# Kernel optimization log

Measured on AMD Instinct MI355X. Metric: run time of the kernel, lower is better.

The kernel has to match this reference:

```python
import jax, jax.numpy as jnp
import numpy as np

# ---- straight-through binary quantizers (custom VJP matches torch autograd.Functions) ----
@jax.custom_vjp
def bq(x):
    return jnp.sign(x)
def _bq_fwd(x):
    return jnp.sign(x), x
def _bq_bwd(x, g):
    return (g * ((x > -1.0) & (x < 1.0)).astype(g.dtype),)
bq.defvjp(_bq_fwd, _bq_bwd)

@jax.custom_vjp
def bq_quad(x):
    return jnp.sign(x)
def _bqq_fwd(x):
    return jnp.sign(x), x
def _bqq_bwd(x, g):
    return (jnp.maximum(2.0 - jnp.abs(2.0 * x), 0.0) * g,)
bq_quad.defvjp(_bqq_fwd, _bqq_bwd)

def bilinear(x, W, s, b):
    # BiLinear: row-centered sign weights scaled by learned per-row factor, sign activations
    Wc = W - jnp.mean(W, axis=-1, keepdims=True)
    Wb = s * bq(Wc)                      # (out, in)
    return bq(x) @ Wb.T + b

def selective_scan(u, delta, A, Bs, Cs, D, delta_bias):
    # u, delta: (B,K,Dn,L); A: (K,Dn,N); Bs,Cs: (B,K,N,L); D, delta_bias: (K,Dn)
    Bn, K, Dn, L = u.shape
    N = A.shape[-1]
    delta = jax.nn.softplus(delta + delta_bias[None, :, :, None])
    def step(h, inp):
        ut, dt, Bt, Ct = inp             # (B,K,Dn),(B,K,Dn),(B,K,N),(B,K,N)
        dA = jnp.exp(dt[..., None] * A[None])
        h = dA * h + (dt * ut)[..., None] * Bt[:, :, None, :]
        y = jnp.einsum('bkdn,bkn->bkd', h, Ct)
        return h, y
    h0 = jnp.zeros((Bn, K, Dn, N), u.dtype)
    _, ys = jax.lax.scan(step, h0,
                         (u.transpose(3, 0, 1, 2), delta.transpose(3, 0, 1, 2),
                          Bs.transpose(3, 0, 1, 2), Cs.transpose(3, 0, 1, 2)))
    y = ys.transpose(1, 2, 3, 0)         # (B,K,Dn,L)
    return y + D[None, :, :, None] * u

def _forward(x, W_in, b_in, s_in, move0_b, conv_W, conv_b, rp_b0, prelu_a, rp_b1,
             Wl, bl, sl, Wd, bd, sd, dt_bias, A_logs, Ds, ln_w, ln_b, W_out, b_out, s_out):
    Bn, H, Wi, dm = x.shape
    Dn = conv_W.shape[0]
    K = 4
    N = A_logs.shape[1]
    R = Wd.shape[2]
    L = H * Wi
    xz = bilinear(x, W_in, s_in, b_in)                  # (B,H,W,2*Dn)
    xp, z = jnp.split(xz, 2, axis=-1)
    xc = xp.transpose(0, 3, 1, 2)                       # (B,Dn,H,W)
    # BConv2d: move0 bias -> sign (quad STE) -> binary conv -> RPReLU -> residual
    t = bq_quad(xc + move0_b[None, :, None, None])
    sc = jax.lax.stop_gradient(jnp.mean(jnp.abs(conv_W), axis=(1, 2, 3), keepdims=True))
    cw = jnp.clip(conv_W, -1.0, 1.0)
    Wb = jax.lax.stop_gradient(sc * jnp.sign(conv_W) - cw) + cw
    t = jax.lax.conv_general_dilated(t, Wb, (1, 1), [(1, 1), (1, 1)],
                                     dimension_numbers=('NCHW', 'OIHW', 'NCHW'))
    t = t + conv_b[None, :, None, None]
    t = t + rp_b0[None, :, None, None]
    t = jnp.where(t >= 0, t, prelu_a[None, :, None, None] * t)
    t = t + rp_b1[None, :, None, None] + xc
    xconv = jax.nn.silu(t)
    # 4-direction scan inputs
    x_flat = xconv.reshape(Bn, Dn, L)
    x_tr = xconv.transpose(0, 1, 3, 2).reshape(Bn, Dn, L)
    x_hwwh = jnp.stack([x_flat, x_tr], axis=1)
    xs = jnp.concatenate([x_hwwh, jnp.flip(x_hwwh, axis=-1)], axis=1)   # (B,K,Dn,L)
    # NOTE: torch does .view(B,L,-1) on contiguous (B,Dn,L) slices = raw reshape (not transpose)
    xin = xs.reshape(Bn, K, L, Dn)
    x_dbl = jax.vmap(bilinear, in_axes=(1, 0, 0, 0), out_axes=1)(xin, Wl, sl, bl)  # (B,K,L,R+2N)
    x_dbl = x_dbl.transpose(0, 1, 3, 2)                                 # (B,K,R+2N,L)
    dts_r, Bs, Cs = jnp.split(x_dbl, [R, R + N], axis=2)
    dts_in = dts_r.reshape(Bn, K, L, R)  # raw reshape, matches torch .view
    dts = jax.vmap(bilinear, in_axes=(1, 0, 0, 0), out_axes=1)(dts_in, Wd, sd, bd)  # (B,K,L,Dn)
    dts = dts.transpose(0, 1, 3, 2)                                     # (B,K,Dn,L)
    A = -jnp.exp(A_logs).reshape(K, Dn, N)
    out_y = selective_scan(xs, dts, A, Bs, Cs, Ds.reshape(K, Dn), dt_bias.reshape(K, Dn))
    inv_y = jnp.flip(out_y[:, 2:4], axis=-1)
    wh_y = out_y[:, 1].reshape(Bn, Dn, Wi, H).transpose(0, 1, 3, 2).reshape(Bn, Dn, L)
    invwh_y = inv_y[:, 1].reshape(Bn, Dn, Wi, H).transpose(0, 1, 3, 2).reshape(Bn, Dn, L)
    y = out_y[:, 0] + inv_y[:, 0] + wh_y + invwh_y                      # (B,Dn,L)
    y = y.transpose(0, 2, 1).reshape(Bn, H, Wi, Dn)
    mu = jnp.mean(y, axis=-1, keepdims=True)
    var = jnp.var(y, axis=-1, keepdims=True)
    y = (y - mu) / jnp.sqrt(var + 1e-5) * ln_w + ln_b                   # LayerNorm eps=1e-5
    y = y * jax.nn.silu(z)
    return bilinear(y, W_out, s_out, b_out)

def setup_inputs():
    key = jax.random.key(0)
    ks = jax.random.split(key, 12)
    B, H, Wi, dm = 4, 64, 64, 96
    Dn, N, R, K = 192, 16, 6, 4
    u = lambda k, sh, a: jax.random.uniform(k, sh, jnp.float32, -a, a)
    x = jax.random.normal(ks[0], (B, H, Wi, dm), jnp.float32)
    W_in = u(ks[1], (2 * Dn, dm), 0.015)
    b_in = u(ks[2], (2 * Dn,), 0.01)
    s_in = jnp.mean(jnp.abs(W_in), axis=1, keepdims=True)
    move0_b = jnp.zeros((Dn,), jnp.float32)
    conv_W = 0.05 * jax.random.normal(ks[3], (Dn, Dn, 3, 3), jnp.float32)
    conv_b = u(ks[4], (Dn,), 0.01)
    rp_b0 = jnp.zeros((Dn,), jnp.float32)
    prelu_a = 0.25 * jnp.ones((Dn,), jnp.float32)
    rp_b1 = jnp.zeros((Dn,), jnp.float32)
    Wl = u(ks[5], (K, R + 2 * N, Dn), 0.015)
    bl = u(ks[6], (K, R + 2 * N), 0.01)
    sl = jnp.mean(jnp.abs(Wl), axis=2, keepdims=True)
    std = R ** -0.5
    Wd = u(ks[7], (K, Dn, R), std)
    bd = u(ks[8], (K, Dn), 0.01)
    sd = jnp.mean(jnp.abs(Wd), axis=2, keepdims=True)
    dt = jnp.exp(jax.random.uniform(ks[9], (K * Dn,), jnp.float32)
                 * (np.log(0.1) - np.log(0.001)) + np.log(0.001))
    dt = jnp.clip(dt, 1e-4, None)
    dt_bias = dt + jnp.log(-jnp.expm1(-dt))
    A_logs = jnp.tile(jnp.log(jnp.arange(1, N + 1, dtype=jnp.float32))[None, :], (K * Dn, 1))
    Ds = jnp.ones((K * Dn,), jnp.float32)
    ln_w = jnp.ones((Dn,), jnp.float32)
    ln_b = jnp.zeros((Dn,), jnp.float32)
    W_out = u(ks[10], (dm, Dn), 0.015)
    b_out = u(ks[11], (dm,), 0.01)
    s_out = jnp.mean(jnp.abs(W_out), axis=1, keepdims=True)
    return dict(x=x, W_in=W_in, b_in=b_in, s_in=s_in, move0_b=move0_b, conv_W=conv_W,
                conv_b=conv_b, rp_b0=rp_b0, prelu_a=prelu_a, rp_b1=rp_b1, Wl=Wl, bl=bl,
                sl=sl, Wd=Wd, bd=bd, sd=sd, dt_bias=dt_bias, A_logs=A_logs, Ds=Ds,
                ln_w=ln_w, ln_b=ln_b, W_out=W_out, b_out=b_out, s_out=s_out)

def reference(x, W_in, b_in, s_in, move0_b, conv_W, conv_b, rp_b0, prelu_a, rp_b1,
              Wl, bl, sl, Wd, bd, sd, dt_bias, A_logs, Ds, ln_w, ln_b, W_out, b_out, s_out):
    return _forward(x, W_in, b_in, s_in, move0_b, conv_W, conv_b, rp_b0, prelu_a, rp_b1,
                    Wl, bl, sl, Wd, bd, sd, dt_bias, A_logs, Ds, ln_w, ln_b, W_out, b_out, s_out)
```

## Files before the change

kernel.cpp:

```cpp
#include <hip/hip_runtime.h>
#include <math.h>
#include <stdint.h>

#define BB 4
#define HH 64
#define WW2 64
#define DM 96
#define DN 192
#define KK 4
#define NN 16
#define RR 6
#define LL 4096
#define RN 38

#define LOG2E 1.4426950408889634f
#define LN2   0.6931471805599453f

#define OFF_WDB      0
#define OFF_WCS      4608
#define OFF_WAUX     15360
#define OFF_WSC      16896
#define OFF_WBIB     17088
#define OFF_WOUTB    18240
#define OFF_WLBB     18816
#define OFF_XBP      19728
#define OFF_PXS      19728
#define OFF_XC       412992
#define OFF_ZS       3558720
#define OFF_XCONV    6704448
#define OFF_XS       9850176
#define OFF_SSUM     22433088
#define OFF_HEND     OFF_XCONV

#define PLANE 4356

__device__ __forceinline__ float fsign(float v) {
  return (v > 0.f) ? 1.f : ((v < 0.f) ? -1.f : 0.f);
}
__device__ __forceinline__ float softplusf(float v) {
  return fmaxf(v, 0.f) + LN2 * log2f(1.f + exp2f(-fabsf(v) * LOG2E));
}
__device__ __forceinline__ float siluf(float v) {
  return v / (1.f + expf(-v));
}
__device__ __forceinline__ float waveAllSum(float s) {
  #pragma unroll
  for (int off = 32; off; off >>= 1) s += __shfl_xor(s, off, 64);
  return s;
}

__global__ __launch_bounds__(64) void k_prep(
    const float* __restrict__ W_in, const float* __restrict__ s_in,
    const float* __restrict__ W_out, const float* __restrict__ s_out,
// ... 100 lines not shown
    uint32_t* plane = (uint32_t*)(ws + OFF_XBP) + (size_t)p * PLANE;
    for (int i = lane; i < 66; i += 64) {
      plane[i] = 0u;
      plane[65 * 66 + i] = 0u;
    }
    for (int i = lane; i < 64; i += 64) {
      plane[(i + 1) * 66] = 0u;
      plane[(i + 1) * 66 + 65] = 0u;
    }
  }
}

__global__ __launch_bounds__(384) void k_bilin_in(
    const float* __restrict__ x, const float* __restrict__ b_in,
    const float* __restrict__ s_in, const float* __restrict__ move0,
    const float* __restrict__ ws, float* __restrict__ xc, float* __restrict__ zs,
    uint32_t* __restrict__ xb) {
  __shared__ uint32_t spx[16 * 3];
  __shared__ float sxz[384 * 17];
  __shared__ float smv[DN];
  int p0 = blockIdx.x * 16;
  if (threadIdx.x < 48) {
    int pix = threadIdx.x / 3, wd = threadIdx.x % 3;
    const float* base = x + (size_t)(p0 + pix) * DM + wd * 32;
    uint32_t wv = 0;
    #pragma unroll
    for (int i = 0; i < 32; ++i) wv |= (base[i] > 0.f ? 1u : 0u) << i;
    spx[pix * 3 + wd] = wv;
  }
  if (threadIdx.x < DN) smv[threadIdx.x] = move0[threadIdx.x];
  __syncthreads();
  int o = threadIdx.x;
  uint32_t w0, w1, w2;
  {
    const uint32_t* wb = (const uint32_t*)(ws + OFF_WBIB) + o * 3;
    w0 = wb[0]; w1 = wb[1]; w2 = wb[2];
  }
  float bias = b_in[o], sc = s_in[o];
  #pragma unroll
  for (int pix = 0; pix < 16; ++pix) {
    int P = (int)__popc(spx[pix * 3 + 0] ^ w0) + (int)__popc(spx[pix * 3 + 1] ^ w1) +
            (int)__popc(spx[pix * 3 + 2] ^ w2);
    sxz[o * 17 + pix] = bias + sc * (float)(DM - 2 * P);
  }
  __syncthreads();
  int b = p0 >> 12, l0 = p0 & 4095;
  for (int f = threadIdx.x; f < DN * 16; f += 384) {
    int od = f >> 4, pix = f & 15;
    xc[((size_t)(b * DN + od)) * LL + l0 + pix] = sxz[od * 17 + pix];
  }
  for (int f = threadIdx.x; f < DN * 16; f += 384) {
    int pix = f / DN, oz = f - pix * DN;
    zs[(size_t)(p0 + pix) * DN + oz] = siluf(sxz[(DN + oz) * 17 + pix]);
  }
  if (threadIdx.x < 96) {
    int pix = threadIdx.x / 6, cw = threadIdx.x % 6;
    uint32_t wv = 0;
    #pragma unroll
    for (int i = 0; i < 32; ++i) {
      int dch = cw * 32 + i;
      wv |= ((sxz[dch * 17 + pix] + smv[dch] > 0.f) ? 1u : 0u) << i;
    }
    int l = l0 + pix, h = l >> 6, w = l & 63;
    uint32_t* plane = xb + (size_t)(b * 6 + cw) * PLANE;
    plane[(h + 1) * 66 + 1 + w] = wv;
  }
}

// ... 59 lines not shown
    }
    if (isB) {
      corr += saux[oc * 8 + 3];
      if (isL) corr -= saux[oc * 8 + 6];
      if (isR) corr -= saux[oc * 8 + 7];
    }
    float acc = sconst[oc * 4 + 0] * (float)(1728 - 2 * P + corr);
    float t = acc + sconst[oc * 4 + 1];
    t = (t >= 0.f) ? t : sconst[oc * 4 + 2] * t;
    t += sconst[oc * 4 + 3] + *xcp;
    *xop = siluf(t);
    xcp += LL; xop += LL;
  }
}

__global__ __launch_bounds__(256) void k_build_xs(const float* __restrict__ xconv,
                                                  float* __restrict__ xs,
                                                  uint32_t* __restrict__ pxs) {
  __shared__ float tile[64][65];
  int bd = blockIdx.x;
  int b = bd / DN, d = bd % DN;
  const float* img = xconv + (size_t)bd * LL;
  for (int i = threadIdx.x; i < LL; i += 256)
    tile[i >> 6][i & 63] = img[i];
  __syncthreads();
  int lane = threadIdx.x & 63;
  #pragma unroll
  for (int k = 0; k < 4; ++k) {
    size_t base = ((size_t)((b * KK + k) * DN + d)) * LL;
    for (int j = threadIdx.x; j < LL; j += 256) {
      float v;
      if (k == 0)      v = tile[j >> 6][j & 63];
      else if (k == 1) v = tile[j & 63][j >> 6];
      else if (k == 2) { int t2 = 4095 - j; v = tile[t2 >> 6][t2 & 63]; }
      else             { int t2 = 4095 - j; v = tile[t2 & 63][t2 >> 6]; }
      xs[base + j] = v;
      unsigned long long m = __ballot(v > 0.f);
      if (lane == 0)       pxs[(base + j) >> 5] = (uint32_t)m;
      else if (lane == 32) pxs[(base + j) >> 5] = (uint32_t)(m >> 32);
    }
  }
}

__device__ __forceinline__ void rpowers(float r, float* a) {
  float r2 = r * r, r3 = r2 * r, r4 = r2 * r2, r8 = r4 * r4;
  a[0] = r;       a[1] = r2;      a[2] = r3;      a[3] = r4;
  a[4] = r4 * r;  a[5] = r4 * r2; a[6] = r4 * r3; a[7] = r8;
  a[8] = r8 * r;  a[9] = r8 * r2; a[10] = r8 * r3; a[11] = r8 * r4;
  a[12] = r8 * a[4]; a[13] = r8 * a[5]; a[14] = r8 * a[6]; a[15] = r8 * r8;
}

__global__ __launch_bounds__(192) void k_scan_a(
    const float* __restrict__ xs, const uint32_t* __restrict__ pxs,
    const float* __restrict__ ws, const float* __restrict__ bl,
    const float* __restrict__ sl, const float* __restrict__ bd,
    const float* __restrict__ dt_bias, const float* __restrict__ A_logs,
    float* __restrict__ hend, float* __restrict__ Ssum) {
  int c = blockIdx.x & 63;
  int bk = blockIdx.x >> 6;
  int k = bk & 3;
  int d = threadIdx.x;
  int t0 = c << 6;
  __shared__ uint32_t sdtm[64];
  __shared__ uint32_t spxr[64 * 6];
  __shared__ uint32_t swl[RN * 6];
  __shared__ float sblv[RN], sslv[RN];
  __shared__ float4 sB4[256];
  __shared__ float sDV[7 * 192], sR[7 * 192];
  float* sBf = (float*)sB4;
  const uint32_t* ppx = pxs + (size_t)bk * 24576;
  for (int i = d; i < 384; i += 192) spxr[i] = ppx[t0 * 6 + i];
  for (int i = d; i < RN * 6; i += 192) swl[i] = ((const uint32_t*)(ws + OFF_WLBB))[k * RN * 6 + i];
  if (d < RN) {
    sblv[d] = bl[k * RN + d];
    sslv[d] = sl[k * RN + d];
  }
  __syncthreads();
  if (d < 64) {
    uint32_t m = 0;
    int fbase = (t0 + d) * 6;
    #pragma unroll
    for (int r = 0; r < 6; ++r) {
      int f = fbase + r;
      int o = f >> 12, l = f & 4095;
      const uint32_t* prow = ppx + l * 6;
      int P = 0;
      #pragma unroll
      for (int j = 0; j < 6; ++j) P += (int)__popc(prow[j] ^ swl[o * 6 + j]);
      float val = sblv[o] + sslv[o] * (float)(DN - 2 * P);
      m |= (val > 0.f ? 1u : 0u) << r;
    }
    sdtm[d] = m;
  }
  for (int i = d; i < 1024; i += 192) {
    int t = i >> 4, n = i & 15;
    int o = RR + n;
    int P = 0;
    #pragma unroll
    for (int j = 0; j < 6; ++j) P += (int)__popc(spxr[t * 6 + j] ^ swl[o * 6 + j]);
    sBf[t * 16 + n] = sblv[o] + sslv[o] * (float)(DN - 2 * P);
  }
  uint32_t w6 = ((const uint32_t*)(ws + OFF_WDB))[k * DN + d];
  float sdv = (ws + OFF_WDB)[768 + k * DN + d];
  float biasd = bd[k * DN + d] + dt_bias[k * DN + d];
  #pragma unroll
  for (int pc = 0; pc < 7; ++pc) {
    float dv = softplusf(biasd + sdv * (float)(RR - 2 * pc));
    sDV[pc * 192 + d] = dv;
    sR[pc * 192 + d] = exp2f(-dv * LOG2E);
  }
  float Araw[16];
  bool fok = true;
  {
    const float* ap = A_logs + (k * DN + d) * NN;
    #pragma unroll
    for (int n = 0; n < NN; ++n) {
      Araw[n] = -expf(ap[n]);
      fok = fok && (fabsf(Araw[n] + (float)(n + 1)) < 1e-3f);
    }
  }
  bool fastpath = (__ballot(fok) == ~0ull);
  float h[16];
  #pragma unroll
  for (int n = 0; n < NN; ++n) h[n] = 0.f;
  float S = 0.f;
  const float* up = xs + ((size_t)bk * DN + d) * LL + t0;
  __syncthreads();
  if (fastpath) {
    #pragma unroll 1
    for (int tt = 0; tt < 16; ++tt) {
      float4 u4 = *(const float4*)(up + 4 * tt);
      #pragma unroll
      for (int q = 0; q < 4; ++q) {
        int t = 4 * tt + q;
        float uv = (q == 0) ? u4.x : (q == 1) ? u4.y : (q == 2) ? u4.z : u4.w;
        int pc = (int)__popc(sdtm[t] ^ w6);
        float dv = sDV[pc * 192 + d];
        float rr = sR[pc * 192 + d];
        S += dv;
        float du = dv * uv;
        float a[16];
        rpowers(rr, a);
        #pragma unroll
        for (int g = 0; g < 4; ++g) {
          float4 bv = sB4[t * 4 + g];
          h[4 * g + 0] = a[4 * g + 0] * h[4 * g + 0] + du * bv.x;
          h[4 * g + 1] = a[4 * g + 1] * h[4 * g + 1] + du * bv.y;
          h[4 * g + 2] = a[4 * g + 2] * h[4 * g + 2] + du * bv.z;
          h[4 * g + 3] = a[4 * g + 3] * h[4 * g + 3] + du * bv.w;
        }
      }
    }
  } else {
    float An[16];
    #pragma unroll
    for (int n = 0; n < NN; ++n) An[n] = Araw[n] * LOG2E;
    #pragma unroll 1
    for (int tt = 0; tt < 16; ++tt) {
      float4 u4 = *(const float4*)(up + 4 * tt);
      #pragma unroll
      for (int q = 0; q < 4; ++q) {
        int t = 4 * tt + q;
        float uv = (q == 0) ? u4.x : (q == 1) ? u4.y : (q == 2) ? u4.z : u4.w;
        int pc = (int)__popc(sdtm[t] ^ w6);
        float dv = sDV[pc * 192 + d];
        S += dv;
        float du = dv * uv;
        #pragma unroll
        for (int g = 0; g < 4; ++g) {
          float4 bv = sB4[t * 4 + g];
          float a0 = exp2f(dv * An[4 * g + 0]);
          float a1 = exp2f(dv * An[4 * g + 1]);
          float a2 = exp2f(dv * An[4 * g + 2]);
          float a3 = exp2f(dv * An[4 * g + 3]);
          h[4 * g + 0] = a0 * h[4 * g + 0] + du * bv.x;
          h[4 * g + 1] = a1 * h[4 * g + 1] + du * bv.y;
          h[4 * g + 2] = a2 * h[4 * g + 2] + du * bv.z;
          h[4 * g + 3] = a3 * h[4 * g + 3] + du * bv.w;
        }
      }
    }
  }
  float* hp = hend + (size_t)c * 49152 + (size_t)(bk * DN + d) * 16;
  #pragma unroll
  for (int n = 0; n < NN; n += 4)
    *(float4*)(hp + n) = make_float4(h[n], h[n + 1], h[n + 2], h[n + 3]);
  Ssum[c * 3072 + bk * DN + d] = S;
}

__global__ __launch_bounds__(256) void k_scan_b(
    const float* __restrict__ A_logs, const float* __restrict__ Ssum,
    float* __restrict__ hend) {
  int tid = blockIdx.x * 256 + threadIdx.x;
  int bkd = tid >> 4, n = tid & 15;
  int bk = bkd / DN, d = bkd - bk * DN;
  int k = bk & 3;
  float An2 = -expf(A_logs[(k * DN + d) * NN + n]) * LOG2E;
  float h = 0.f;
  float Sc = Ssum[bkd];
  float he = hend[tid];
  #pragma unroll 1
  for (int c = 0; c < 64; ++c) {
    float Sn = 0.f, hn = 0.f;
    if (c < 63) {
      Sn = Ssum[(c + 1) * 3072 + bkd];
      hn = hend[(size_t)(c + 1) * 49152 + tid];
    }
    hend[(size_t)c * 49152 + tid] = h;
    h = exp2f(An2 * Sc) * h + he;
    Sc = Sn; he = hn;
  }
}

__global__ __launch_bounds__(192) void k_scan_c(
    float* __restrict__ xs, const uint32_t* __restrict__ pxs,
    const float* __restrict__ ws, const float* __restrict__ bl,
    const float* __restrict__ sl, const float* __restrict__ bd,
    const float* __restrict__ dt_bias, const float* __restrict__ A_logs,
    const float* __restrict__ Ds, const float* __restrict__ h0buf) {
  int c = blockIdx.x & 63;
  int bk = blockIdx.x >> 6;
  int k = bk & 3;
  int d = threadIdx.x;
  int t0 = c << 6;
  __shared__ uint32_t sdtm[64];
  __shared__ uint32_t spxr[64 * 6];
  __shared__ uint32_t swl[RN * 6];
  __shared__ float sblv[RN], sslv[RN];
  __shared__ float4 sB4[256];
  __shared__ float4 sC4[256];
  __shared__ float sDV[7 * 192], sR[7 * 192];
  __shared__ float ytile[192 * 17];
  float* sBf = (float*)sB4;
  float* sCf = (float*)sC4;
  const uint32_t* ppx = pxs + (size_t)bk * 24576;
  for (int i = d; i < 384; i += 192) spxr[i] = ppx[t0 * 6 + i];
  for (int i = d; i < RN * 6; i += 192) swl[i] = ((const uint32_t*)(ws + OFF_WLBB))[k * RN * 6 + i];
  if (d < RN) {
    sblv[d] = bl[k * RN + d];
    sslv[d] = sl[k * RN + d];
  }
  __syncthreads();
  if (d < 64) {
    uint32_t m = 0;
    int fbase = (t0 + d) * 6;
    #pragma unroll
    for (int r = 0; r < 6; ++r) {
      int f = fbase + r;
      int o = f >> 12, l = f & 4095;
      const uint32_t* prow = ppx + l * 6;
      int P = 0;
      #pragma unroll
      for (int j = 0; j < 6; ++j) P += (int)__popc(prow[j] ^ swl[o * 6 + j]);
      float val = sblv[o] + sslv[o] * (float)(DN - 2 * P);
      m |= (val > 0.f ? 1u : 0u) << r;
    }
    sdtm[d] = m;
  }
  for (int i = d; i < 2048; i += 192) {
    int t = i >> 5, nn = i & 31;
    int o = RR + nn;
    int P = 0;
    #pragma unroll
    for (int j = 0; j < 6; ++j) P += (int)__popc(spxr[t * 6 + j] ^ swl[o * 6 + j]);
    float val = sblv[o] + sslv[o] * (float)(DN - 2 * P);
    if (nn < 16) sBf[t * 16 + nn] = val;
    else         sCf[t * 16 + (nn - 16)] = val;
  }
  uint32_t w6 = ((const uint32_t*)(ws + OFF_WDB))[k * DN + d];
  float sdv = (ws + OFF_WDB)[768 + k * DN + d];
  float biasd = bd[k * DN + d] + dt_bias[k * DN + d];
  float Dd = Ds[k * DN + d];
  #pragma unroll
  for (int pc = 0; pc < 7; ++pc) {
    float dv = softplusf(biasd + sdv * (float)(RR - 2 * pc));
    sDV[pc * 192 + d] = dv;
    sR[pc * 192 + d] = exp2f(-dv * LOG2E);
  }
  float Araw[16];
  bool fok = true;
  {
    const float* ap = A_logs + (k * DN + d) * NN;
    #pragma unroll
    for (int n = 0; n < NN; ++n) {
      Araw[n] = -expf(ap[n]);
      fok = fok && (fabsf(Araw[n] + (float)(n + 1)) < 1e-3f);
    }
  }
  bool fastpath = (__ballot(fok) == ~0ull);
  float h[16];
  {
    const float* hp = h0buf + (size_t)c * 49152 + (size_t)(bk * DN + d) * 16;
    #pragma unroll
    for (int n = 0; n < NN; n += 4) {
      float4 v = *(const float4*)(hp + n);
      h[n] = v.x; h[n + 1] = v.y; h[n + 2] = v.z; h[n + 3] = v.w;
    }
  }
  float* xbase = xs + ((size_t)bk * DN) * LL;
  const float* up = xbase + (size_t)d * LL + t0;
  float An[16];
  if (!fastpath) {
    #pragma unroll
    for (int n = 0; n < NN; ++n) An[n] = Araw[n] * LOG2E;
  }
  __syncthreads();
  #pragma unroll 1
  for (int seg = 0; seg < 4; ++seg) {
    #pragma unroll 1
    for (int tt = 0; tt < 4; ++tt) {
      float4 u4 = *(const float4*)(up + seg * 16 + 4 * tt);
      #pragma unroll
      for (int q = 0; q < 4; ++q) {
        int t = seg * 16 + 4 * tt + q;
        float uv = (q == 0) ? u4.x : (q == 1) ? u4.y : (q == 2) ? u4.z : u4.w;
        int pc = (int)__popc(sdtm[t] ^ w6);
        float dv = sDV[pc * 192 + d];
        float du = dv * uv;
        float yv = Dd * uv;
        if (fastpath) {
          float rr = sR[pc * 192 + d];
          float a[16];
          rpowers(rr, a);
          #pragma unroll
          for (int g = 0; g < 4; ++g) {
            float4 bv = sB4[t * 4 + g];
            float4 cv = sC4[t * 4 + g];
            h[4 * g + 0] = a[4 * g + 0] * h[4 * g + 0] + du * bv.x;
            h[4 * g + 1] = a[4 * g + 1] * h[4 * g + 1] + du * bv.y;
            h[4 * g + 2] = a[4 * g + 2] * h[4 * g + 2] + du * bv.z;
            h[4 * g + 3] = a[4 * g + 3] * h[4 * g + 3] + du * bv.w;
            yv += cv.x * h[4 * g + 0];
            yv += cv.y * h[4 * g + 1];
            yv += cv.z * h[4 * g + 2];
            yv += cv.w * h[4 * g + 3];
          }
        } else {
          #pragma unroll
          for (int g = 0; g < 4; ++g) {
            float4 bv = sB4[t * 4 + g];
            float4 cv = sC4[t * 4 + g];
            float a0 = exp2f(dv * An[4 * g + 0]);
            float a1 = exp2f(dv * An[4 * g + 1]);
            float a2 = exp2f(dv * An[4 * g + 2]);
            float a3 = exp2f(dv * An[4 * g + 3]);
            h[4 * g + 0] = a0 * h[4 * g + 0] + du * bv.x;
            h[4 * g + 1] = a1 * h[4 * g + 1] + du * bv.y;
            h[4 * g + 2] = a2 * h[4 * g + 2] + du * bv.z;
            h[4 * g + 3] = a3 * h[4 * g + 3] + du * bv.w;
            yv += cv.x * h[4 * g + 0];
            yv += cv.y * h[4 * g + 1];
            yv += cv.z * h[4 * g + 2];
            yv += cv.w * h[4 * g + 3];
          }
        }
        ytile[d * 17 + (t & 15)] = yv;
      }
    }
    __syncthreads();
    for (int i = d; i < 3072; i += 192) {
      int dd = i >> 4, tq = i & 15;
      xbase[(size_t)dd * LL + t0 + seg * 16 + tq] = ytile[dd * 17 + tq];
    }
    __syncthreads();
  }
}

__global__ __launch_bounds__(256) void k_comb(const float* __restrict__ xs,
                                              float* __restrict__ y) {
  __shared__ float tA[64][65], tB[64][65];
  int bd = blockIdx.x;
  int b = bd / DN, d = bd % DN;
  const float* p0 = xs + ((size_t)((b * 4 + 0) * DN + d)) * LL;
  const float* p1 = xs + ((size_t)((b * 4 + 1) * DN + d)) * LL;
  const float* p2 = xs + ((size_t)((b * 4 + 2) * DN + d)) * LL;
  const float* p3 = xs + ((size_t)((b * 4 + 3) * DN + d)) * LL;
  for (int i = threadIdx.x; i < LL; i += 256) {
    tA[i >> 6][i & 63] = p1[i];
    tB[i >> 6][i & 63] = p3[i];
  }
  __syncthreads();
  float* yo = y + (size_t)bd * LL;
  for (int l = threadIdx.x; l < LL; l += 256) {
    float v = p0[l] + tA[l & 63][l >> 6] + p2[4095 - l] +
              tB[63 - (l & 63)][63 - (l >> 6)];
    yo[l] = v;
  }
}

__global__ __launch_bounds__(256) void k_ln_out(
    const float* __restrict__ y, const float* __restrict__ zs,
    const float* __restrict__ ln_w, const float* __restrict__ ln_b,
    const float* __restrict__ ws, const float* __restrict__ b_out,
    const float* __restrict__ s_out, float* __restrict__ out) {
  __shared__ float ty[64 * 193];
  __shared__ float ps[256];
  __shared__ float smu[64], srs[64];
  __shared__ float slw[DN], slb[DN];
  __shared__ uint32_t ybits[64 * 6];
  __shared__ uint32_t swo[96 * 6];
  __shared__ float sb[96], ssc[96];
  int b = blockIdx.x >> 6;
  int l0 = (blockIdx.x & 63) << 6;
  const float* yp = y + (size_t)b * DN * LL + l0;
  if (threadIdx.x < DN) {
    slw[threadIdx.x] = ln_w[threadIdx.x];
    slb[threadIdx.x] = ln_b[threadIdx.x];
  }
  for (int i = threadIdx.x; i < 96 * 6; i += 256) swo[i] = ((const uint32_t*)(ws + OFF_WOUTB))[i];
  if (threadIdx.x < 96) {
    sb[threadIdx.x] = b_out[threadIdx.x];
    ssc[threadIdx.x] = s_out[threadIdx.x];
  }
  for (int i = threadIdx.x; i < 64 * DN; i += 256) {
    int d2 = i >> 6, lc = i & 63;
    ty[lc * 193 + d2] = yp[(size_t)d2 * LL + lc];
  }
  __syncthreads();
  int lc = threadIdx.x & 63, part = threadIdx.x >> 6;
  float s = 0.f;
  for (int d = part * 48; d < part * 48 + 48; ++d) s += ty[lc * 193 + d];
  ps[threadIdx.x] = s;
  __syncthreads();
  if (threadIdx.x < 64)
    smu[threadIdx.x] = (ps[threadIdx.x] + ps[threadIdx.x + 64] +
                        ps[threadIdx.x + 128] + ps[threadIdx.x + 192]) / (float)DN;
  __syncthreads();
  float mu = smu[lc];
  float q = 0.f;
  for (int d = part * 48; d < part * 48 + 48; ++d) {
    float v = ty[lc * 193 + d] - mu; q += v * v;
  }
  ps[threadIdx.x] = q;
  __syncthreads();
  if (threadIdx.x < 64) {
    float var = (ps[threadIdx.x] + ps[threadIdx.x + 64] +
                 ps[threadIdx.x + 128] + ps[threadIdx.x + 192]) / (float)DN;
    srs[threadIdx.x] = rsqrtf(var + 1e-5f);
  }
  __syncthreads();
  for (int item = threadIdx.x; item < 64 * 6; item += 256) {
    int lc2 = item / 6, wd = item % 6;
    float mu2 = smu[lc2], rs2 = srs[lc2];
    const float* zb = zs + (size_t)(b * LL + l0 + lc2) * DN + wd * 32;
    uint32_t wv = 0;
    #pragma unroll
    for (int i = 0; i < 32; ++i) {
      int d = wd * 32 + i;
      float ln = (ty[lc2 * 193 + d] - mu2) * rs2 * slw[d] + slb[d];
      wv |= ((ln * zb[i] > 0.f) ? 1u : 0u) << i;
    }
    ybits[lc2 * 6 + wd] = wv;
  }
  __syncthreads();
  float* op = out + (size_t)(b * LL + l0) * DM;
  for (int oi = threadIdx.x; oi < 64 * DM; oi += 256) {
    int pr = oi / DM, m = oi % DM;
    int P = 0;
    #pragma unroll
    for (int j = 0; j < 6; ++j) P += (int)__popc(ybits[pr * 6 + j] ^ swo[m * 6 + j]);
    op[(size_t)pr * DM + m] = sb[m] + ssc[m] * (float)(DN - 2 * P);
  }
}

extern "C" void kernel_launch(void* const* d_in, const int* in_sizes, int n_in,
// ... 17 lines not shown
  const float* sd      = (const float*)d_in[15];
  const float* dt_bias = (const float*)d_in[16];
  const float* A_logs  = (const float*)d_in[17];
  const float* Ds      = (const float*)d_in[18];
  const float* ln_w    = (const float*)d_in[19];
  const float* ln_b    = (const float*)d_in[20];
  const float* W_out   = (const float*)d_in[21];
  const float* b_out   = (const float*)d_in[22];
  const float* s_out   = (const float*)d_in[23];
  float* ws  = (float*)d_ws;
  float* out = (float*)d_out;

  hipLaunchKernelGGL(k_prep, dim3(1616), dim3(64), 0, stream,
                     W_in, s_in, W_out, s_out, Wl, sl, Wd, sd, conv_W, ws);
  hipLaunchKernelGGL(k_bilin_in, dim3(1024), dim3(384), 0, stream,
                     x, b_in, s_in, move0_b, ws, ws + OFF_XC, ws + OFF_ZS,
                     (uint32_t*)(ws + OFF_XBP));
  hipLaunchKernelGGL(k_conv, dim3(256), dim3(256), 0, stream,
                     (const uint32_t*)(ws + OFF_XBP), ws + OFF_XC,
                     (const uint32_t*)(ws + OFF_WCS), (const int*)(ws + OFF_WAUX),
                     ws + OFF_WSC, conv_b, rp_b0, prelu_a, rp_b1,
                     ws + OFF_XCONV);
  hipLaunchKernelGGL(k_build_xs, dim3(768), dim3(256), 0, stream,
                     ws + OFF_XCONV, ws + OFF_XS, (uint32_t*)(ws + OFF_PXS));
  hipLaunchKernelGGL(k_scan_a, dim3(1024), dim3(192), 0, stream,
                     ws + OFF_XS, (const uint32_t*)(ws + OFF_PXS), ws, bl, sl,
                     bd, dt_bias, A_logs, ws + OFF_HEND, ws + OFF_SSUM);
  hipLaunchKernelGGL(k_scan_b, dim3(192), dim3(256), 0, stream,
                     A_logs, ws + OFF_SSUM, ws + OFF_HEND);
  hipLaunchKernelGGL(k_scan_c, dim3(1024), dim3(192), 0, stream,
                     ws + OFF_XS, (const uint32_t*)(ws + OFF_PXS), ws, bl, sl,
                     bd, dt_bias, A_logs, Ds, ws + OFF_HEND);
  hipLaunchKernelGGL(k_comb, dim3(768), dim3(256), 0, stream,
                     ws + OFF_XS, ws + OFF_XC);
  hipLaunchKernelGGL(k_ln_out, dim3(256), dim3(256), 0, stream,
                     ws + OFF_XC, ws + OFF_ZS, ln_w, ln_b, ws, b_out, s_out, out);
}
```

Measured before the change: 311.9 us.

## Restructure chunked scan to compute local outputs in pass A and add correction pass

```diff
diff --git a/kernel.cpp b/kernel.cpp
--- a/kernel.cpp
+++ b/kernel.cpp
@@ -25,18 +25,18 @@
 #define OFF_WLBB     18816
 #define OFF_XBP      19728
 #define OFF_PXS      19728
-#define OFF_XC       412992
-#define OFF_ZS       3558720
-#define OFF_XCONV    6704448
-#define OFF_XS       9850176
-#define OFF_SSUM     22433088
-#define OFF_HEND     OFF_XCONV
+#define OFF_PXIN     412944
+#define OFF_XP       462096
+#define OFF_XCONV    3607824
+#define OFF_XCT      6753552
+#define OFF_HEND     462096
+#define OFF_YA       9899280
+#define OFF_SSUM     22482192
 
 #define PLANE 4356
-
-__device__ __forceinline__ float fsign(float v) {
-  return (v > 0.f) ? 1.f : ((v < 0.f) ? -1.f : 0.f);
-}
+#define NCH 128
+#define CHUNK 32
+
 __device__ __forceinline__ float softplusf(float v) {
   return fmaxf(v, 0.f) + LN2 * log2f(1.f + exp2f(-fabsf(v) * LOG2E));
 }
@@ -167,10 +167,10 @@
 __global__ __launch_bounds__(384) void k_bilin_in(
     const float* __restrict__ x, const float* __restrict__ b_in,
     const float* __restrict__ s_in, const float* __restrict__ move0,
-    const float* __restrict__ ws, float* __restrict__ xc, float* __restrict__ zs,
-    uint32_t* __restrict__ xb) {
+    const float* __restrict__ ws, float* __restrict__ xp,
+    uint32_t* __restrict__ pxin, uint32_t* __restrict__ xb) {
   __shared__ uint32_t spx[16 * 3];
-  __shared__ float sxz[384 * 17];
+  __shared__ float sxz[192 * 17];
   __shared__ float smv[DN];
   int p0 = blockIdx.x * 16;
   if (threadIdx.x < 48) {
@@ -183,7 +183,8 @@
   }
   if (threadIdx.x < DN) smv[threadIdx.x] = move0[threadIdx.x];
   __syncthreads();
-  int o = threadIdx.x;
+  int half = threadIdx.x / 192;
+  int o = threadIdx.x - half * 192;
   uint32_t w0, w1, w2;
   {
     const uint32_t* wb = (const uint32_t*)(ws + OFF_WBIB) + o * 3;
@@ -191,7 +192,8 @@
   }
   float bias = b_in[o], sc = s_in[o];
   #pragma unroll
-  for (int pix = 0; pix < 16; ++pix) {
+  for (int pp = 0; pp < 8; ++pp) {
+    int pix = half * 8 + pp;
     int P = (int)__popc(spx[pix * 3 + 0] ^ w0) + (int)__popc(spx[pix * 3 + 1] ^ w1) +
             (int)__popc(spx[pix * 3 + 2] ^ w2);
     sxz[o * 17 + pix] = bias + sc * (float)(DM - 2 * P);
@@ -200,11 +202,11 @@
   int b = p0 >> 12, l0 = p0 & 4095;
   for (int f = threadIdx.x; f < DN * 16; f += 384) {
     int od = f >> 4, pix = f & 15;
-    xc[((size_t)(b * DN + od)) * LL + l0 + pix] = sxz[od * 17 + pix];
-  }
-  for (int f = threadIdx.x; f < DN * 16; f += 384) {
-    int pix = f / DN, oz = f - pix * DN;
-    zs[(size_t)(p0 + pix) * DN + oz] = siluf(sxz[(DN + oz) * 17 + pix]);
+    xp[((size_t)(b * DN + od)) * LL + l0 + pix] = sxz[od * 17 + pix];
+  }
+  if (threadIdx.x < 48) {
+    int pix = threadIdx.x / 3, wd = threadIdx.x % 3;
+    pxin[(size_t)(p0 + pix) * 3 + wd] = spx[pix * 3 + wd];
   }
   if (threadIdx.x < 96) {
     int pix = threadIdx.x / 6, cw = threadIdx.x % 6;
@@ -294,12 +296,11 @@
   }
 }
 
-__global__ __launch_bounds__(256) void k_build_xs(const float* __restrict__ xconv,
-                                                  float* __restrict__ xs,
-                                                  uint32_t* __restrict__ pxs) {
+__global__ __launch_bounds__(256) void k_build_bits(const float* __restrict__ xconv,
+                                                    uint32_t* __restrict__ pxs) {
   __shared__ float tile[64][65];
   int bd = blockIdx.x;
-  int b = bd / DN, d = bd % DN;
+  int b = bd / DN, dch = bd - b * DN;
   const float* img = xconv + (size_t)bd * LL;
   for (int i = threadIdx.x; i < LL; i += 256)
     tile[i >> 6][i & 63] = img[i];
@@ -307,18 +308,36 @@
   int lane = threadIdx.x & 63;
   #pragma unroll
   for (int k = 0; k < 4; ++k) {
-    size_t base = ((size_t)((b * KK + k) * DN + d)) * LL;
+    size_t wbase = ((size_t)((b * KK + k) * DN + dch)) * 128;
     for (int j = threadIdx.x; j < LL; j += 256) {
       float v;
       if (k == 0)      v = tile[j >> 6][j & 63];
       else if (k == 1) v = tile[j & 63][j >> 6];
       else if (k == 2) { int t2 = 4095 - j; v = tile[t2 >> 6][t2 & 63]; }
       else             { int t2 = 4095 - j; v = tile[t2 & 63][t2 >> 6]; }
-      xs[base + j] = v;
       unsigned long long m = __ballot(v > 0.f);
-      if (lane == 0)       pxs[(base + j) >> 5] = (uint32_t)m;
-      else if (lane == 32) pxs[(base + j) >> 5] = (uint32_t)(m >> 32);
-    }
+      if (lane == 0)       pxs[wbase + (j >> 5)] = (uint32_t)m;
+      else if (lane == 32) pxs[wbase + (j >> 5)] = (uint32_t)(m >> 32);
+    }
+  }
+}
+
+__global__ __launch_bounds__(256) void k_xpose(const float* __restrict__ xconv,
+                                               float* __restrict__ xct) {
+  __shared__ float tile[64][65];
+  int ts = blockIdx.x & 63;
+  int rest = blockIdx.x >> 6;
+  int dg = rest % 3;
+  int b = rest / 3;
+  int d0 = dg * 64, t0 = ts * 64;
+  for (int i = threadIdx.x; i < 4096; i += 256) {
+    int dd = i >> 6, tt = i & 63;
+    tile[dd][tt] = xconv[((size_t)(b * DN + d0 + dd)) * LL + t0 + tt];
+  }
+  __syncthreads();
+  for (int i = threadIdx.x; i < 4096; i += 256) {
+    int tt = i >> 6, dd = i & 63;
+    xct[((size_t)(b * LL + t0 + tt)) * DN + d0 + dd] = tile[dd][tt];
   }
 }
 
@@ -331,32 +350,35 @@
 }
 
 __global__ __launch_bounds__(192) void k_scan_a(
-    const float* __restrict__ xs, const uint32_t* __restrict__ pxs,
+    const float* __restrict__ xct, const uint32_t* __restrict__ pxs,
     const float* __restrict__ ws, const float* __restrict__ bl,
     const float* __restrict__ sl, const float* __restrict__ bd,
     const float* __restrict__ dt_bias, const float* __restrict__ A_logs,
+    const float* __restrict__ Ds, float* __restrict__ yA,
     float* __restrict__ hend, float* __restrict__ Ssum) {
-  int c = blockIdx.x & 63;
-  int bk = blockIdx.x >> 6;
-  int k = bk & 3;
+  int c = blockIdx.x & (NCH - 1);
+  int bk = blockIdx.x >> 7;
+  int k = bk & 3, b = bk >> 2;
   int d = threadIdx.x;
-  int t0 = c << 6;
-  __shared__ uint32_t sdtm[64];
-  __shared__ uint32_t spxr[64 * 6];
+  int t0 = c << 5;
+  __shared__ uint32_t sdtm[CHUNK];
+  __shared__ uint32_t spxr[CHUNK * 6];
   __shared__ uint32_t swl[RN * 6];
   __shared__ float sblv[RN], sslv[RN];
-  __shared__ float4 sB4[256];
+  __shared__ float4 sB4[CHUNK * 4];
+  __shared__ float4 sC4[CHUNK * 4];
   __shared__ float sDV[7 * 192], sR[7 * 192];
   float* sBf = (float*)sB4;
+  float* sCf = (float*)sC4;
   const uint32_t* ppx = pxs + (size_t)bk * 24576;
-  for (int i = d; i < 384; i += 192) spxr[i] = ppx[t0 * 6 + i];
+  spxr[d] = ppx[t0 * 6 + d];
   for (int i = d; i < RN * 6; i += 192) swl[i] = ((const uint32_t*)(ws + OFF_WLBB))[k * RN * 6 + i];
   if (d < RN) {
     sblv[d] = bl[k * RN + d];
     sslv[d] = sl[k * RN + d];
   }
   __syncthreads();
-  if (d < 64) {
+  if (d < CHUNK) {
     uint32_t m = 0;
     int fbase = (t0 + d) * 6;
     #pragma unroll
@@ -372,17 +394,20 @@
     }
     sdtm[d] = m;
   }
-  for (int i = d; i < 1024; i += 192) {
-    int t = i >> 4, n = i & 15;
-    int o = RR + n;
+  for (int i = d; i < CHUNK * 32; i += 192) {
+    int t = i >> 5, nn = i & 31;
+    int o = RR + nn;
     int P = 0;
     #pragma unroll
     for (int j = 0; j < 6; ++j) P += (int)__popc(spxr[t * 6 + j] ^ swl[o * 6 + j]);
-    sBf[t * 16 + n] = sblv[o] + sslv[o] * (float)(DN - 2 * P);
+    float val = sblv[o] + sslv[o] * (float)(DN - 2 * P);
+    if (nn < 16) sBf[t * 16 + nn] = val;
+    else         sCf[t * 16 + (nn - 16)] = val;
   }
   uint32_t w6 = ((const uint32_t*)(ws + OFF_WDB))[k * DN + d];
   float sdv = (ws + OFF_WDB)[768 + k * DN + d];
   float biasd = bd[k * DN + d] + dt_bias[k * DN + d];
+  float Dd = Ds[k * DN + d];
   #pragma unroll
   for (int pc = 0; pc < 7; ++pc) {
     float dv = softplusf(biasd + sdv * (float)(RR - 2 * pc));
@@ -400,55 +425,61 @@
     }
   }
   bool fastpath = (__ballot(fok) == ~0ull);
+  float An[16];
+  if (!fastpath) {
+    #pragma unroll
+    for (int n = 0; n < NN; ++n) An[n] = Araw[n] * LOG2E;
+  }
   float h[16];
   #pragma unroll
   for (int n = 0; n < NN; ++n) h[n] = 0.f;
   float S = 0.f;
-  const float* up = xs + ((size_t)bk * DN + d) * LL + t0;
-  __syncthreads();
-  if (fastpath) {
-    #pragma unroll 1
-    for (int tt = 0; tt < 16; ++tt) {
-      float4 u4 = *(const float4*)(up + 4 * tt);
-      #pragma unroll
-      for (int q = 0; q < 4; ++q) {
-        int t = 4 * tt + q;
-        float uv = (q == 0) ? u4.x : (q == 1) ? u4.y : (q == 2) ? u4.z : u4.w;
-        int pc = (int)__popc(sdtm[t] ^ w6);
-        float dv = sDV[pc * 192 + d];
-        float rr = sR[pc * 192 + d];
-        S += dv;
-        float du = dv * uv;
+  int ubase = b * (LL * DN) + d;
+  int ybase = bk * (LL * DN) + d;
+  __syncthreads();
+  #pragma unroll 1
+  for (int seg = 0; seg < 4; ++seg) {
+    float uu[8];
+    int r192[8];
+    #pragma unroll
+    for (int i = 0; i < 8; ++i) {
+      int t = t0 + seg * 8 + i;
+      int r = (k >= 2) ? (4095 - t) : t;
+      if (k & 1) r = ((r & 63) << 6) | (r >> 6);
+      r192[i] = r * DN;
+      uu[i] = xct[ubase + r192[i]];
+    }
+    #pragma unroll
+    for (int i = 0; i < 8; ++i) {
+      int t = seg * 8 + i;
+      float uv = uu[i];
+      int pc = (int)__popc(sdtm[t] ^ w6);
+      float dv = sDV[pc * 192 + d];
+      S += dv;
+      float du = dv * uv;
+      float yv = Dd * uv;
+      if (fastpath) {
+        float rv = sR[pc * 192 + d];
         float a[16];
-        rpowers(rr, a);
+        rpowers(rv, a);
         #pragma unroll
         for (int g = 0; g < 4; ++g) {
           float4 bv = sB4[t * 4 + g];
+          float4 cv = sC4[t * 4 + g];
           h[4 * g + 0] = a[4 * g + 0] * h[4 * g + 0] + du * bv.x;
           h[4 * g + 1] = a[4 * g + 1] * h[4 * g + 1] + du * bv.y;
           h[4 * g + 2] = a[4 * g + 2] * h[4 * g + 2] + du * bv.z;
           h[4 * g + 3] = a[4 * g + 3] * h[4 * g + 3] + du * bv.w;
+          yv += cv.x * h[4 * g + 0];
+          yv += cv.y * h[4 * g + 1];
+          yv += cv.z * h[4 * g + 2];
+          yv += cv.w * h[4 * g + 3];
         }
-      }
-    }
-  } else {
-    float An[16];
-    #pragma unroll
-    for (int n = 0; n < NN; ++n) An[n] = Araw[n] * LOG2E;
-    #pragma unroll 1
-    for (int tt = 0; tt < 16; ++tt) {
-      float4 u4 = *(const float4*)(up + 4 * tt);
-      #pragma unroll
-      for (int q = 0; q < 4; ++q) {
-        int t = 4 * tt + q;
-        float uv = (q == 0) ? u4.x : (q == 1) ? u4.y : (q == 2) ? u4.z : u4.w;
-        int pc = (int)__popc(sdtm[t] ^ w6);
-        float dv = sDV[pc * 192 + d];
-        S += dv;
-        float du = dv * uv;
+      } else {
         #pragma unroll
         for (int g = 0; g < 4; ++g) {
           float4 bv = sB4[t * 4 + g];
+          float4 cv = sC4[t * 4 + g];
           float a0 = exp2f(dv * An[4 * g + 0]);
           float a1 = exp2f(dv * An[4 * g + 1]);
           float a2 = exp2f(dv * An[4 * g + 2]);
@@ -457,8 +488,13 @@
           h[4 * g + 1] = a1 * h[4 * g + 1] + du * bv.y;
           h[4 * g + 2] = a2 * h[4 * g + 2] + du * bv.z;
           h[4 * g + 3] = a3 * h[4 * g + 3] + du * bv.w;
+          yv += cv.x * h[4 * g + 0];
+          yv += cv.y * h[4 * g + 1];
+          yv += cv.z * h[4 * g + 2];
+          yv += cv.w * h[4 * g + 3];
         }
       }
+      yA[ybase + r192[i]] = yv;
     }
   }
   float* hp = hend + (size_t)c * 49152 + (size_t)(bk * DN + d) * 16;
@@ -480,9 +516,9 @@
   float Sc = Ssum[bkd];
   float he = hend[tid];
   #pragma unroll 1
-  for (int c = 0; c < 64; ++c) {
+  for (int c = 0; c < NCH; ++c) {
     float Sn = 0.f, hn = 0.f;
-    if (c < 63) {
+    if (c < NCH - 1) {
       Sn = Ssum[(c + 1) * 3072 + bkd];
       hn = hend[(size_t)(c + 1) * 49152 + tid];
     }
@@ -492,36 +528,34 @@
   }
 }
 
-__global__ __launch_bounds__(192) void k_scan_c(
-    float* __restrict__ xs, const uint32_t* __restrict__ pxs,
+__global__ __launch_bounds__(192) void k_scan_corr(
+    float* __restrict__ yA, const uint32_t* __restrict__ pxs,
     const float* __restrict__ ws, const float* __restrict__ bl,
     const float* __restrict__ sl, const float* __restrict__ bd,
     const float* __restrict__ dt_bias, const float* __restrict__ A_logs,
-    const float* __restrict__ Ds, const float* __restrict__ h0buf) {
-  int c = blockIdx.x & 63;
-  int bk = blockIdx.x >> 6;
+    const float* __restrict__ h0buf) {
+  int c = blockIdx.x & (NCH - 1);
+  if (c == 0) return;
+  int bk = blockIdx.x >> 7;
   int k = bk & 3;
   int d = threadIdx.x;
-  int t0 = c << 6;
-  __shared__ uint32_t sdtm[64];
-  __shared__ uint32_t spxr[64 * 6];
+  int t0 = c << 5;
+  __shared__ uint32_t sdtm[CHUNK];
+  __shared__ uint32_t spxr[CHUNK * 6];
   __shared__ uint32_t swl[RN * 6];
   __shared__ float sblv[RN], sslv[RN];
-  __shared__ float4 sB4[256];
-  __shared__ float4 sC4[256];
-  __shared__ float sDV[7 * 192], sR[7 * 192];
-  __shared__ float ytile[192 * 17];
-  float* sBf = (float*)sB4;
+  __shared__ float4 sC4[CHUNK * 4];
+  __shared__ float sDV[7 * 192];
   float* sCf = (float*)sC4;
   const uint32_t* ppx = pxs + (size_t)bk * 24576;
-  for (int i = d; i < 384; i += 192) spxr[i] = ppx[t0 * 6 + i];
+  spxr[d] = ppx[t0 * 6 + d];
   for (int i = d; i < RN * 6; i += 192) swl[i] = ((const uint32_t*)(ws + OFF_WLBB))[k * RN * 6 + i];
   if (d < RN) {
     sblv[d] = bl[k * RN + d];
     sslv[d] = sl[k * RN + d];
   }
   __syncthreads();
-  if (d < 64) {
+  if (d < CHUNK) {
     uint32_t m = 0;
     int fbase = (t0 + d) * 6;
     #pragma unroll
@@ -537,26 +571,20 @@
     }
     sdtm[d] = m;
   }
-  for (int i = d; i < 2048; i += 192) {
-    int t = i >> 5, nn = i & 31;
-    int o = RR + nn;
+  for (int i = d; i < CHUNK * 16; i += 192) {
+    int t = i >> 4, n = i & 15;
+    int o = RR + NN + n;
     int P = 0;
     #pragma unroll
     for (int j = 0; j < 6; ++j) P += (int)__popc(spxr[t * 6 + j] ^ swl[o * 6 + j]);
-    float val = sblv[o] + sslv[o] * (float)(DN - 2 * P);
-    if (nn < 16) sBf[t * 16 + nn] = val;
-    else         sCf[t * 16 + (nn - 16)] = val;
+    sCf[t * 16 + n] = sblv[o] + sslv[o] * (float)(DN - 2 * P);
   }
   uint32_t w6 = ((const uint32_t*)(ws + OFF_WDB))[k * DN + d];
   float sdv = (ws + OFF_WDB)[768 + k * DN + d];
   float biasd = bd[k * DN + d] + dt_bias[k * DN + d];
-  float Dd = Ds[k * DN + d];
   #pragma unroll
-  for (int pc = 0; pc < 7; ++pc) {
-    float dv = softplusf(biasd + sdv * (float)(RR - 2 * pc));
-    sDV[pc * 192 + d] = dv;
-    sR[pc * 192 + d] = exp2f(-dv * LOG2E);
-  }
+  for (int pc = 0; pc < 7; ++pc)
+    sDV[pc * 192 + d] = softplusf(biasd + sdv * (float)(RR - 2 * pc));
   float Araw[16];
   bool fok = true;
   {
@@ -568,108 +596,71 @@
     }
   }
   bool fastpath = (__ballot(fok) == ~0ull);
-  float h[16];
+  float An[16];
+  if (!fastpath) {
+    #pragma unroll
+    for (int n = 0; n < NN; ++n) An[n] = Araw[n] * LOG2E;
+  }
+  float h0[16];
   {
     const float* hp = h0buf + (size_t)c * 49152 + (size_t)(bk * DN + d) * 16;
     #pragma unroll
     for (int n = 0; n < NN; n += 4) {
       float4 v = *(const float4*)(hp + n);
-      h[n] = v.x; h[n + 1] = v.y; h[n + 2] = v.z; h[n + 3] = v.w;
-    }
-  }
-  float* xbase = xs + ((size_t)bk * DN) * LL;
-  const float* up = xbase + (size_t)d * LL + t0;
-  float An[16];
-  if (!fastpath) {
-    #pragma unroll
-    for (int n = 0; n < NN; ++n) An[n] = Araw[n] * LOG2E;
-  }
+      h0[n] = v.x; h0[n + 1] = v.y; h0[n + 2] = v.z; h0[n + 3] = v.w;
+    }
+  }
+  float S = 0.f;
+  int ybase = bk * (LL * DN) + d;
   __syncthreads();
   #pragma unroll 1
   for (int seg = 0; seg < 4; ++seg) {
-    #pragma unroll 1
-    for (int tt = 0; tt < 4; ++tt) {
-      float4 u4 = *(const float4*)(up + seg * 16 + 4 * tt);
-      #pragma unroll
-      for (int q = 0; q < 4; ++q) {
-        int t = seg * 16 + 4 * tt + q;
-        float uv = (q == 0) ? u4.x : (q == 1) ? u4.y : (q == 2) ? u4.z : u4.w;
-        int pc = (int)__popc(sdtm[t] ^ w6);
-        float dv = sDV[pc * 192 + d];
-        float du = dv * uv;
-        float yv = Dd * uv;
-        if (fastpath) {
-          float rr = sR[pc * 192 + d];
-          float a[16];
-          rpowers(rr, a);
-          #pragma unroll
-          for (int g = 0; g < 4; ++g) {
-            float4 bv = sB4[t * 4 + g];
-            float4 cv = sC4[t * 4 + g];
-            h[4 * g + 0] = a[4 * g + 0] * h[4 * g + 0] + du * bv.x;
-            h[4 * g + 1] = a[4 * g + 1] * h[4 * g + 1] + du * bv.y;
-            h[4 * g + 2] = a[4 * g + 2] * h[4 * g + 2] + du * bv.z;
-            h[4 * g + 3] = a[4 * g + 3] * h[4 * g + 3] + du * bv.w;
-            yv += cv.x * h[4 * g + 0];
-            yv += cv.y * h[4 * g + 1];
-            yv += cv.z * h[4 * g + 2];
-            yv += cv.w * h[4 * g + 3];
-          }
-        } else {
-          #pragma unroll
-          for (int g = 0; g < 4; ++g) {
-            float4 bv = sB4[t * 4 + g];
-            float4 cv = sC4[t * 4 + g];
-            float a0 = exp2f(dv * An[4 * g + 0]);
-            float a1 = exp2f(dv * An[4 * g + 1]);
-            float a2 = exp2f(dv * An[4 * g + 2]);
-            float a3 = exp2f(dv * An[4 * g + 3]);
-            h[4 * g + 0] = a0 * h[4 * g + 0] + du * bv.x;
-            h[4 * g + 1] = a1 * h[4 * g + 1] + du * bv.y;
-            h[4 * g + 2] = a2 * h[4 * g + 2] + du * bv.z;
-            h[4 * g + 3] = a3 * h[4 * g + 3] + du * bv.w;
-            yv += cv.x * h[4 * g + 0];
-            yv += cv.y * h[4 * g + 1];
-            yv += cv.z * h[4 * g + 2];
-            yv += cv.w * h[4 * g + 3];
-          }
+    float yy[8];
+    int r192[8];
+    #pragma unroll
+    for (int i = 0; i < 8; ++i) {
+      int t = t0 + seg * 8 + i;
+      int r = (k >= 2) ? (4095 - t) : t;
+      if (k & 1) r = ((r & 63) << 6) | (r >> 6);
+      r192[i] = r * DN;
+      yy[i] = yA[ybase + r192[i]];
+    }
+    #pragma unroll
+    for (int i = 0; i < 8; ++i) {
+      int t = seg * 8 + i;
+      int pc = (int)__popc(sdtm[t] ^ w6);
+      S += sDV[pc * 192 + d];
+      float yv = 0.f;
+      if (fastpath) {
+        float rho = exp2f(-S * LOG2E);
+        float a[16];
+        rpowers(rho, a);
+        #pragma unroll
+        for (int g = 0; g < 4; ++g) {
+          float4 cv = sC4[t * 4 + g];
+          yv += cv.x * (a[4 * g + 0] * h0[4 * g + 0]);
+          yv += cv.y * (a[4 * g + 1] * h0[4 * g + 1]);
+          yv += cv.z * (a[4 * g + 2] * h0[4 * g + 2]);
+          yv += cv.w * (a[4 * g + 3] * h0[4 * g + 3]);
         }
-        ytile[d * 17 + (t & 15)] = yv;
+      } else {
+        #pragma unroll
+        for (int g = 0; g < 4; ++g) {
+          float4 cv = sC4[t * 4 + g];
+          yv += cv.x * (exp2f(S * An[4 * g + 0]) * h0[4 * g + 0]);
+          yv += cv.y * (exp2f(S * An[4 * g + 1]) * h0[4 * g + 1]);
+          yv += cv.z * (exp2f(S * An[4 * g + 2]) * h0[4 * g + 2]);
+          yv += cv.w * (exp2f(S * An[4 * g + 3]) * h0[4 * g + 3]);
+        }
       }
-    }
-    __syncthreads();
-    for (int i = d; i < 3072; i += 192) {
-      int dd = i >> 4, tq = i & 15;
-      xbase[(size_t)dd * LL + t0 + seg * 16 + tq] = ytile[dd * 17 + tq];
-    }
-    __syncthreads();
-  }
-}
-
-__global__ __launch_bounds__(256) void k_comb(const float* __restrict__ xs,
-                                              float* __restrict__ y) {
-  __shared__ float tA[64][65], tB[64][65];
-  int bd = blockIdx.x;
-  int b = bd / DN, d = bd % DN;
-  const float* p0 = xs + ((size_t)((b * 4 + 0) * DN + d)) * LL;
-  const float* p1 = xs + ((size_t)((b * 4 + 1) * DN + d)) * LL;
-  const float* p2 = xs + ((size_t)((b * 4 + 2) * DN + d)) * LL;
-  const float* p3 = xs + ((size_t)((b * 4 + 3) * DN + d)) * LL;
-  for (int i = threadIdx.x; i < LL; i += 256) {
-    tA[i >> 6][i & 63] = p1[i];
-    tB[i >> 6][i & 63] = p3[i];
-  }
-  __syncthreads();
-  float* yo = y + (size_t)bd * LL;
-  for (int l = threadIdx.x; l < LL; l += 256) {
-    float v = p0[l] + tA[l & 63][l >> 6] + p2[4095 - l] +
-              tB[63 - (l & 63)][63 - (l >> 6)];
-    yo[l] = v;
+      yA[ybase + r192[i]] = yy[i] + yv;
+    }
   }
 }
 
 __global__ __launch_bounds__(256) void k_ln_out(
-    const float* __restrict__ y, const float* __restrict__ zs,
+    const float* __restrict__ yA, const uint32_t* __restrict__ pxin,
+    const float* __restrict__ b_in, const float* __restrict__ s_in,
     const float* __restrict__ ln_w, const float* __restrict__ ln_b,
     const float* __restrict__ ws, const float* __restrict__ b_out,
     const float* __restrict__ s_out, float* __restrict__ out) {
@@ -680,21 +671,32 @@
   __shared__ uint32_t ybits[64 * 6];
   __shared__ uint32_t swo[96 * 6];
   __shared__ float sb[96], ssc[96];
+  __shared__ uint32_t szw[DN * 3];
+  __shared__ float szb[DN], szs[DN];
+  __shared__ uint32_t spxt[64 * 3];
   int b = blockIdx.x >> 6;
   int l0 = (blockIdx.x & 63) << 6;
-  const float* yp = y + (size_t)b * DN * LL + l0;
   if (threadIdx.x < DN) {
     slw[threadIdx.x] = ln_w[threadIdx.x];
     slb[threadIdx.x] = ln_b[threadIdx.x];
+    szb[threadIdx.x] = b_in[DN + threadIdx.x];
+    szs[threadIdx.x] = s_in[DN + threadIdx.x];
   }
   for (int i = threadIdx.x; i < 96 * 6; i += 256) swo[i] = ((const uint32_t*)(ws + OFF_WOUTB))[i];
+  for (int i = threadIdx.x; i < DN * 3; i += 256) szw[i] = ((const uint32_t*)(ws + OFF_WBIB))[DN * 3 + i];
   if (threadIdx.x < 96) {
     sb[threadIdx.x] = b_out[threadIdx.x];
     ssc[threadIdx.x] = s_out[threadIdx.x];
   }
+  for (int i = threadIdx.x; i < 192; i += 256) spxt[i] = pxin[(size_t)(b * LL + l0) * 3 + i];
+  const float* y0 = yA + (size_t)(b * 4 + 0) * (LL * DN) + (size_t)l0 * DN;
+  const float* y1 = yA + (size_t)(b * 4 + 1) * (LL * DN) + (size_t)l0 * DN;
+  const float* y2 = yA + (size_t)(b * 4 + 2) * (LL * DN) + (size_t)l0 * DN;
+  const float* y3 = yA + (size_t)(b * 4 + 3) * (LL * DN) + (size_t)l0 * DN;
   for (int i = threadIdx.x; i < 64 * DN; i += 256) {
-    int d2 = i >> 6, lc = i & 63;
-    ty[lc * 193 + d2] = yp[(size_t)d2 * LL + lc];
+    int lc = i / DN, dd = i - lc * DN;
+    size_t off = (size_t)lc * DN + dd;
+    ty[lc * 193 + dd] = y0[off] + y1[off] + y2[off] + y3[off];
   }
   __syncthreads();
   int lc = threadIdx.x & 63, part = threadIdx.x >> 6;
@@ -720,15 +722,18 @@
   }
   __syncthreads();
   for (int item = threadIdx.x; item < 64 * 6; item += 256) {
-    int lc2 = item / 6, wd = item % 6;
+    int lc2 = item / 6, wd = item - (item / 6) * 6;
     float mu2 = smu[lc2], rs2 = srs[lc2];
-    const float* zb = zs + (size_t)(b * LL + l0 + lc2) * DN + wd * 32;
+    uint32_t px0 = spxt[lc2 * 3 + 0], px1 = spxt[lc2 * 3 + 1], px2 = spxt[lc2 * 3 + 2];
     uint32_t wv = 0;
     #pragma unroll
     for (int i = 0; i < 32; ++i) {
-      int d = wd * 32 + i;
-      float ln = (ty[lc2 * 193 + d] - mu2) * rs2 * slw[d] + slb[d];
-      wv |= ((ln * zb[i] > 0.f) ? 1u : 0u) << i;
+      int dd = wd * 32 + i;
+      float lnv = (ty[lc2 * 193 + dd] - mu2) * rs2 * slw[dd] + slb[dd];
+      int P = (int)__popc(px0 ^ szw[dd * 3 + 0]) + (int)__popc(px1 ^ szw[dd * 3 + 1]) +
+              (int)__popc(px2 ^ szw[dd * 3 + 2]);
+      float zv = szb[dd] + szs[dd] * (float)(DM - 2 * P);
+      wv |= ((lnv * zv > 0.f) ? 1u : 0u) << i;
     }
     ybits[lc2 * 6 + wd] = wv;
   }
@@ -776,25 +781,27 @@
   hipLaunchKernelGGL(k_prep, dim3(1616), dim3(64), 0, stream,
                      W_in, s_in, W_out, s_out, Wl, sl, Wd, sd, conv_W, ws);
   hipLaunchKernelGGL(k_bilin_in, dim3(1024), dim3(384), 0, stream,
-                     x, b_in, s_in, move0_b, ws, ws + OFF_XC, ws + OFF_ZS,
-                     (uint32_t*)(ws + OFF_XBP));
+                     x, b_in, s_in, move0_b, ws, ws + OFF_XP,
+                     (uint32_t*)(ws + OFF_PXIN), (uint32_t*)(ws + OFF_XBP));
   hipLaunchKernelGGL(k_conv, dim3(256), dim3(256), 0, stream,
-                     (const uint32_t*)(ws + OFF_XBP), ws + OFF_XC,
+                     (const uint32_t*)(ws + OFF_XBP), ws + OFF_XP,
                      (const uint32_t*)(ws + OFF_WCS), (const int*)(ws + OFF_WAUX),
                      ws + OFF_WSC, conv_b, rp_b0, prelu_a, rp_b1,
                      ws + OFF_XCONV);
-  hipLaunchKernelGGL(k_build_xs, dim3(768), dim3(256), 0, stream,
-                     ws + OFF_XCONV, ws + OFF_XS, (uint32_t*)(ws + OFF_PXS));
-  hipLaunchKernelGGL(k_scan_a, dim3(1024), dim3(192), 0, stream,
-                     ws + OFF_XS, (const uint32_t*)(ws + OFF_PXS), ws, bl, sl,
-                     bd, dt_bias, A_logs, ws + OFF_HEND, ws + OFF_SSUM);
+  hipLaunchKernelGGL(k_build_bits, dim3(768), dim3(256), 0, stream,
+                     ws + OFF_XCONV, (uint32_t*)(ws + OFF_PXS));
+  hipLaunchKernelGGL(k_xpose, dim3(768), dim3(256), 0, stream,
+                     ws + OFF_XCONV, ws + OFF_XCT);
+  hipLaunchKernelGGL(k_scan_a, dim3(2048), dim3(192), 0, stream,
+                     ws + OFF_XCT, (const uint32_t*)(ws + OFF_PXS), ws, bl, sl,
+                     bd, dt_bias, A_logs, Ds, ws + OFF_YA, ws + OFF_HEND,
+                     ws + OFF_SSUM);
   hipLaunchKernelGGL(k_scan_b, dim3(192), dim3(256), 0, stream,
                      A_logs, ws + OFF_SSUM, ws + OFF_HEND);
-  hipLaunchKernelGGL(k_scan_c, dim3(1024), dim3(192), 0, stream,
-                     ws + OFF_XS, (const uint32_t*)(ws + OFF_PXS), ws, bl, sl,
-                     bd, dt_bias, A_logs, Ds, ws + OFF_HEND);
-  hipLaunchKernelGGL(k_comb, dim3(768), dim3(256), 0, stream,
-                     ws + OFF_XS, ws + OFF_XC);
+  hipLaunchKernelGGL(k_scan_corr, dim3(2048), dim3(192), 0, stream,
+                     ws + OFF_YA, (const uint32_t*)(ws + OFF_PXS), ws, bl, sl,
+                     bd, dt_bias, A_logs, ws + OFF_HEND);
   hipLaunchKernelGGL(k_ln_out, dim3(256), dim3(256), 0, stream,
-                     ws + OFF_XC, ws + OFF_ZS, ln_w, ln_b, ws, b_out, s_out, out);
-}
+                     ws + OFF_YA, (const uint32_t*)(ws + OFF_PXIN), b_in, s_in,
+                     ln_w, ln_b, ws, b_out, s_out, out);
+}
```

New measurement: 324.7 us. 1.04x slower.
